# Optimization experiments

Hardware: AMD Instinct MI355X
Metric: run time of the kernel (lower is better)

The kernel has to match this reference:

```python
import jax, jax.numpy as jnp
import numpy as np

N_E = 2048; N_U = 4096; N_SVC = 1024; K = 16; EMB = 8; ED = 8; TH = 16; FD = 32; TK = 3; LVL = 10; B = 8192
DIL = (1, 2, 1, 2)


def setup_inputs() -> dict:
    key = jax.random.key(0)
    ks = list(jax.random.split(key, 64))
    nrm = lambda i, shape, s=0.05: s * jax.random.normal(ks[i], shape, jnp.float32)
    inp = {}
    inp["edge"] = jax.random.normal(ks[0], (1, K, N_E, 11), jnp.float32)
    inp["load"] = jax.random.uniform(ks[1], (1, K, N_E, 3), dtype=jnp.float32)
    inp["svc_tot"] = jax.random.uniform(ks[2], (1, K, N_E, 3), dtype=jnp.float32)
    inp["tra"] = jax.random.normal(ks[3], (1, K, N_U, 4), jnp.float32)
    uid = jax.random.randint(ks[4], (B,), 0, N_U)
    eid = jax.random.randint(ks[5], (B,), 0, N_E)
    sid = jax.random.randint(ks[6], (B,), 0, N_SVC)
    tim = jax.random.randint(ks[7], (B,), 0, K)
    inp["info"] = jnp.stack([uid, eid, sid, tim], -1)[None].astype(jnp.int32)
    inp["srv_attr"] = jnp.concatenate([jnp.arange(N_E)[:, None], jax.random.randint(ks[8], (N_E, 3), 0, LVL)], -1).astype(jnp.int32)
    inp["svc_attr"] = jnp.concatenate([jnp.arange(N_SVC)[:, None], jax.random.randint(ks[9], (N_SVC, 3), 0, LVL)], -1).astype(jnp.int32)
    # --- parameters ---
    inp["usr_tab"] = nrm(10, (N_U, EMB), 1.0)
    inp["srv_tab0"] = nrm(11, (N_E, EMB), 1.0)
    inp["srv_lvl_tabs"] = nrm(12, (3, LVL, EMB), 1.0)
    inp["svc_tab0"] = nrm(13, (N_SVC, EMB), 1.0)
    inp["svc_lvl_tabs"] = nrm(14, (3, LVL, EMB), 1.0)
    inp["lstm_Wih"] = nrm(15, (4 * TH, EMB + 4), 0.2)
    inp["lstm_Whh"] = nrm(16, (4 * TH, TH), 0.2)
    inp["lstm_bih"] = jnp.zeros((4 * TH,), jnp.float32)
    inp["lstm_bhh"] = jnp.zeros((4 * TH,), jnp.float32)
    inp["E1_p"] = nrm(17, (ED, ED, ED), 0.3)
    inp["E2_p"] = nrm(18, (K, ED), 0.01)
    inp["pe_p_W"] = nrm(19, (ED, 11), 0.2)
    inp["pe_p_b"] = jnp.zeros((ED,), jnp.float32)
    inp["E1_a"] = nrm(20, (ED, ED, ED), 0.3)
    inp["E2_a"] = nrm(21, (K, ED), 0.01)
    inp["pe_a_W"] = nrm(22, (ED, 11), 0.2)
    inp["pe_a_b"] = jnp.zeros((ED,), jnp.float32)
    inp["proj_p_W"] = nrm(23, (FD, 3), 0.3)
    inp["proj_p_b"] = jnp.zeros((FD,), jnp.float32)
    inp["proj_a_W"] = nrm(24, (FD, 3), 0.3)
    inp["proj_a_b"] = jnp.zeros((FD,), jnp.float32)
    inp["Wt_p"] = nrm(25, (4, TK, FD, FD), 0.1)
    inp["bt_p"] = jnp.zeros((4, FD), jnp.float32)
    inp["Wg_p"] = nrm(26, (4, FD, FD), 0.1)
    inp["bg_p"] = jnp.zeros((4, FD), jnp.float32)
    inp["Wt_a"] = nrm(27, (4, TK, FD, FD), 0.1)
    inp["bt_a"] = jnp.zeros((4, FD), jnp.float32)
    inp["Wg_a"] = nrm(28, (4, FD, FD), 0.1)
    inp["bg_a"] = jnp.zeros((4, FD), jnp.float32)
    dims = [TH + EMB * 4 * 2 + FD, 64, 32, 16, 8, 4, 1]  # 112 -> ... -> 1
    for i in range(6):
        inp[f"qW{i}"] = nrm(29 + i, (dims[i + 1], dims[i]), 0.1)
        inp[f"qb{i}"] = jnp.zeros((dims[i + 1],), jnp.float32)
    return inp


def _lstm_last(x, Wih, Whh, bih, bhh):
    # x: [n_u, k, in]; returns last hidden state [n_u, TH]
    H = Whh.shape[1]
    def step(carry, xt):
        h, c = carry
        g = xt @ Wih.T + h @ Whh.T + bih + bhh
        i, f, gg, o = jnp.split(g, 4, axis=-1)  # torch gate order i,f,g,o
        c = jax.nn.sigmoid(f) * c + jax.nn.sigmoid(i) * jnp.tanh(gg)
        h = jax.nn.sigmoid(o) * jnp.tanh(c)
        return (h, c), None
    h0 = jnp.zeros((x.shape[0], H), x.dtype)
    (h, _), _ = jax.lax.scan(step, (h0, h0), jnp.swapaxes(x, 0, 1))
    return h


def _adj(ep, E1, E2):
    # einsum('ouv,to,tiu,tjv->tij') factored for efficiency
    M = jnp.einsum('to,ouv->tuv', E2, E1)          # [k, ed, ed]
    T = jnp.einsum('tiu,tuv->tiv', ep, M)          # [k, N, ed]
    S = jnp.einsum('tiv,tjv->tij', T, ep)          # [k, N, N]
    return jax.nn.softmax(jax.nn.relu(S), axis=-1)


def _stream(x, A, Wt, bt, Wg, bg):
    # x: [1, k, N, F]; A: [k, N, N]. Dilated causal temporal conv + graph conv per layer.
    nk = x.shape[1]
    for i, dd in enumerate(DIL):
        pad = (TK - 1) * dd
        xp = jnp.pad(x, ((0, 0), (pad, 0), (0, 0), (0, 0)))
        y = bt[i] + sum(jnp.einsum('btnf,fg->btng', jax.lax.dynamic_slice_in_dim(xp, j * dd, nk, 1), Wt[i, j]) for j in range(TK))
        y = jax.nn.relu(y)
        y = jnp.einsum('btnf,tnm->btmf', y, A)     # per-timestep graph conv
        x = jax.nn.relu(jnp.einsum('btnf,fg->btng', y, Wg[i]) + bg[i])
    return x[:, -1]  # [1, N, F]


def _forward(edge, load, svc_tot, tra, usr_tab, srv_tab0, srv_lvl_tabs, svc_tab0, svc_lvl_tabs,
             lstm_Wih, lstm_Whh, lstm_bih, lstm_bhh,
             E1_p, E2_p, pe_p_W, pe_p_b, E1_a, E2_a, pe_a_W, pe_a_b,
             proj_p_W, proj_p_b, proj_a_W, proj_a_b,
             Wt_p, bt_p, Wg_p, bg_p, Wt_a, bt_a, Wg_a, bg_a,
             qW0, qb0, qW1, qb1, qW2, qb2, qW3, qb3, qW4, qb4, qW5, qb5,
             info, srv_attr, svc_attr):
    edge = edge[0]; loadx = load[0]; svcx = svc_tot[0]; trax = tra[0]; infox = info[0]
    k, n_u = trax.shape[0], trax.shape[1]
    usr_emb = usr_tab[:n_u]                                      # arange lookup
    srv_emb = jnp.concatenate([srv_tab0[srv_attr[:, 0]], srv_lvl_tabs[0][srv_attr[:, 1]],
                               srv_lvl_tabs[1][srv_attr[:, 2]], srv_lvl_tabs[2][srv_attr[:, 3]]], -1)
    svc_emb = jnp.concatenate([svc_tab0[svc_attr[:, 0]], svc_lvl_tabs[0][svc_attr[:, 1]],
                               svc_lvl_tabs[1][svc_attr[:, 2]], svc_lvl_tabs[2][svc_attr[:, 3]]], -1)
    x = jnp.concatenate([jnp.broadcast_to(usr_emb[None], (k, n_u, usr_emb.shape[-1])), trax], -1)
    tra_feat = _lstm_last(jnp.swapaxes(x, 0, 1), lstm_Wih, lstm_Whh, lstm_bih, lstm_bhh)  # [n_u, TH]
    ep = edge @ pe_p_W.T + pe_p_b
    ea = edge @ pe_a_W.T + pe_a_b
    A_p = _adj(ep, E1_p, E2_p)
    A_a = _adj(ea, E1_a, E2_a)
    xp = (loadx @ proj_p_W.T + proj_p_b)[None]   # [1, k, N, FD]
    xa = (svcx @ proj_a_W.T + proj_a_b)[None]
    fp = _stream(xp, A_p, Wt_p, bt_p, Wg_p, bg_p)
    fa = _stream(xa, A_a, Wt_a, bt_a, Wg_a, bg_a)
    srv_fea = (0.5 * (fp + fa))[0]               # mean over stacked streams -> [N, FD]
    h = jnp.concatenate([tra_feat[infox[:, 0]], srv_fea[infox[:, 1]], srv_emb[infox[:, 1]], svc_emb[infox[:, 2]]], -1)
    for W, b in ((qW0, qb0), (qW1, qb1), (qW2, qb2), (qW3, qb3), (qW4, qb4)):
        h = jax.nn.relu(h @ W.T + b)
    return h @ qW5.T + qb5                        # [b, 1]


def reference(edge, load, svc_tot, tra, info, srv_attr, svc_attr, usr_tab, srv_tab0, srv_lvl_tabs, svc_tab0, svc_lvl_tabs,
              lstm_Wih, lstm_Whh, lstm_bih, lstm_bhh,
              E1_p, E2_p, pe_p_W, pe_p_b, E1_a, E2_a, pe_a_W, pe_a_b,
              proj_p_W, proj_p_b, proj_a_W, proj_a_b,
              Wt_p, bt_p, Wg_p, bg_p, Wt_a, bt_a, Wg_a, bg_a,
              qW0, qb0, qW1, qb1, qW2, qb2, qW3, qb3, qW4, qb4, qW5, qb5):
    return _forward(edge, load, svc_tot, tra, usr_tab, srv_tab0, srv_lvl_tabs, svc_tab0, svc_lvl_tabs,
                    lstm_Wih, lstm_Whh, lstm_bih, lstm_bhh,
                    E1_p, E2_p, pe_p_W, pe_p_b, E1_a, E2_a, pe_a_W, pe_a_b,
                    proj_p_W, proj_p_b, proj_a_W, proj_a_b,
                    Wt_p, bt_p, Wg_p, bg_p, Wt_a, bt_a, Wg_a, bg_a,
                    qW0, qb0, qW1, qb1, qW2, qb2, qW3, qb3, qW4, qb4, qW5, qb5,
                    info, srv_attr, svc_attr)
```

## Files before the change

### kernel.cpp

```cpp
#include <hip/hip_runtime.h>
#include <math.h>

#define N_E 2048
#define N_U 4096
#define N_SVC 1024
#define KT 16
#define STRX (KT*N_E*32)
#define YSTR (KT*N_E*32)
#define TSTR (KT*8*N_E)

typedef __attribute__((ext_vector_type(8))) short short8;
typedef __attribute__((ext_vector_type(4))) float f32x4;

__device__ __forceinline__ float sigf(float x){ return 1.0f/(1.0f+__expf(-x)); }
__device__ __forceinline__ float tanhfast(float x){ return 1.0f - 2.0f/(__expf(2.0f*x)+1.0f); }
__device__ __forceinline__ short f2bf(float f){
  union { float f; unsigned u; } x; x.f = f;
  unsigned r = x.u + 0x7FFFu + ((x.u >> 16) & 1u);
  return (short)(r >> 16);
}
__device__ __forceinline__ float bf2f(unsigned short u){
  union { unsigned u; float f; } x; x.u = ((unsigned)u) << 16; return x.f;
}
__device__ __forceinline__ float expm1t(float d){
  float t = fmaf(d, 1.f/24.f, 1.f/6.f);
  t = fmaf(d, t, 0.5f);
  t = fmaf(d, t, 1.f);
  return d*t;
}

__global__ void k_embed(const int* __restrict__ srv_attr, const int* __restrict__ svc_attr,
                        const float* __restrict__ srv_tab0, const float* __restrict__ srv_lvl,
                        const float* __restrict__ svc_tab0, const float* __restrict__ svc_lvl,
                        float* __restrict__ srv_emb, float* __restrict__ svc_emb) {
  int idx = blockIdx.x*256 + threadIdx.x;
  int r = idx >> 5, c = idx & 31;
  int seg = c >> 3, cc = c & 7;
  if (r < N_E) {
    int a = srv_attr[r*4 + seg];
    srv_emb[r*32 + c] = (seg==0) ? srv_tab0[a*8+cc] : srv_lvl[((seg-1)*10 + a)*8 + cc];
  } else {
    int r2 = r - N_E;
    if (r2 < N_SVC) {
      int a = svc_attr[r2*4 + seg];
      svc_emb[r2*32 + c] = (seg==0) ? svc_tab0[a*8+cc] : svc_lvl[((seg-1)*10 + a)*8 + cc];
    }
  }
}

__global__ __launch_bounds__(256) void k_lstm(const float* __restrict__ usr_tab, const float* __restrict__ tra,
                       const float* __restrict__ Wih, const float* __restrict__ Whh,
                       const float* __restrict__ bih, const float* __restrict__ bhh,
                       float* __restrict__ tra_feat) {
  __shared__ float sWih[64*12];
  __shared__ float sWhh[64*16];
  __shared__ float sB[64];
  int tid = threadIdx.x;
  for (int i = tid; i < 64*12; i += 256) sWih[i] = Wih[i];
  for (int i = tid; i < 64*16; i += 256) sWhh[i] = Whh[i];
  if (tid < 64) sB[tid] = bih[tid] + bhh[tid];
  __syncthreads();
  int j  = tid & 15;
  int u  = blockIdx.x*16 + (tid >> 4);
  float xe[8];
  #pragma unroll
  for (int k=0;k<8;k++) xe[k] = usr_tab[u*8+k];
  float h = 0.f, c = 0.f;
  for (int t=0;t<KT;t++) {
    float gi = sB[j], gf = sB[16+j], gg = sB[32+j], go = sB[48+j];
    #pragma unroll
    for (int k=0;k<8;k++) {
      float v = xe[k];
      gi += sWih[j*12+k]*v;      gf += sWih[(16+j)*12+k]*v;
      gg += sWih[(32+j)*12+k]*v; go += sWih[(48+j)*12+k]*v;
    }
    #pragma unroll
    for (int k=0;k<4;k++) {
      float v = tra[((size_t)t*N_U + u)*4 + k];
      gi += sWih[j*12+8+k]*v;      gf += sWih[(16+j)*12+8+k]*v;
      gg += sWih[(32+j)*12+8+k]*v; go += sWih[(48+j)*12+8+k]*v;
    }
    #pragma unroll
    for (int jj=0;jj<16;jj++) {
      float hv = __shfl(h, jj, 16);
      gi += sWhh[j*16+jj]*hv;      gf += sWhh[(16+j)*16+jj]*hv;
      gg += sWhh[(32+j)*16+jj]*hv; go += sWhh[(48+j)*16+jj]*hv;
    }
    c = sigf(gf)*c + sigf(gi)*tanhfast(gg);
    h = sigf(go)*tanhfast(c);
  }
  tra_feat[u*16 + j] = h;
}

__global__ __launch_bounds__(256) void k_peT(const float* __restrict__ edge,
                    const float* __restrict__ Wp, const float* __restrict__ bp,
                    const float* __restrict__ Wa, const float* __restrict__ ba,
                    const float* __restrict__ E1p, const float* __restrict__ E2p,
                    const float* __restrict__ E1a, const float* __restrict__ E2a,
                    float* __restrict__ epp, float* __restrict__ epa,
                    float* __restrict__ Ttp, float* __restrict__ Tta) {
  __shared__ float sM[64];
  __shared__ float sW[88];
  __shared__ float sb[8];
  int s = blockIdx.z, t = 5 + blockIdx.y;
  const float* E1 = s ? E1a : E1p;
  const float* E2 = s ? E2a : E2p;
  const float* W  = s ? Wa : Wp;
  const float* b  = s ? ba : bp;
  float* ep = (s ? epa : epp) + (size_t)t*N_E*8;
  float* Tt = (s ? Tta : Ttp) + (size_t)t*8*N_E;
  int tid = threadIdx.x;
  if (tid < 64) {
    int u = tid >> 3, v = tid & 7;
    float m = 0.f;
    #pragma unroll
    for (int o=0;o<8;o++) m += E2[t*8+o]*E1[(o*8+u)*8+v];
    sM[u*8+v] = m;
  }
  if (tid >= 64 && tid < 152) sW[tid-64] = W[tid-64];
  if (tid >= 152 && tid < 160) sb[tid-152] = b[tid-152];
  __syncthreads();
  int n = blockIdx.x*256 + tid;
  const float* e = edge + ((size_t)t*N_E + n)*11;
  float ev[11];
  #pragma unroll
  for (int k=0;k<11;k++) ev[k] = e[k];
  float epr[8];
  #pragma unroll
  for (int c=0;c<8;c++) {
    float acc = sb[c];
    #pragma unroll
    for (int k=0;k<11;k++) acc = fmaf(ev[k], sW[c*11+k], acc);
    epr[c] = acc;
  }
  float4* eo = (float4*)(ep + (size_t)n*8);
  eo[0] = make_float4(epr[0],epr[1],epr[2],epr[3]);
  eo[1] = make_float4(epr[4],epr[5],epr[6],epr[7]);
  #pragma unroll
  for (int v=0;v<8;v++) {
    float acc = 0.f;
    #pragma unroll
    for (int u=0;u<8;u++) acc = fmaf(epr[u], sM[u*8+v], acc);
    Tt[(size_t)v*N_E + n] = acc;
  }
}

__global__ __launch_bounds__(256) void k_stats(const float* __restrict__ Ttp, const float* __restrict__ Tta,
                        const float* __restrict__ epp, const float* __restrict__ epa,
                        float* __restrict__ partC) {
  __shared__ float sE[256*8];
  int s = blockIdx.z, t = 5 + blockIdx.y;
  int ntile = blockIdx.x & 7, sp = blockIdx.x >> 3;
  int n = ntile*256 + threadIdx.x;
  const float* Tt = (s ? Tta : Ttp) + (size_t)t*8*N_E;
  const float* E = (s ? epa : epp) + (size_t)t*N_E*8;
  int tid = threadIdx.x;
  float tr[8];
  #pragma unroll
  for (int v=0;v<8;v++) tr[v] = Tt[(size_t)v*N_E + n];
  int m0 = sp*256;
  {
    const float4* ge = (const float4*)(E + (size_t)m0*8);
    float4* se = (float4*)sE;
    for (int i = tid; i < 512; i += 256) se[i] = ge[i];
  }
  __syncthreads();
  float qs = 0.f;
  #pragma unroll 4
  for (int m = 0; m < 256; m++) {
    float d = 0.f;
    #pragma unroll
    for (int v=0;v<8;v++) d = fmaf(sE[m*8+v], tr[v], d);
    qs += expm1t(fmaxf(d, 0.f));
  }
  partC[(((size_t)s*KT + t)*8 + sp)*N_E + n] = 256.f + qs;
}

__global__ void k_zinv(const float* __restrict__ partC, float* __restrict__ Z) {
  int i = blockIdx.x*256 + threadIdx.x;
  int n = i & 2047; int stp = i >> 11;
  int s = stp / 11, t = 5 + stp % 11;
  float a = 0.f;
  #pragma unroll
  for (int sp=0;sp<8;sp++) a += partC[(((size_t)s*KT + t)*8 + sp)*N_E + n];
  Z[((size_t)s*KT + t)*N_E + n] = 1.0f/a;
}

__global__ void k_proj(const float* __restrict__ loadx, const float* __restrict__ svcx,
                       const float* __restrict__ Wp, const float* __restrict__ bp,
                       const float* __restrict__ Wa, const float* __restrict__ ba,
                       float* __restrict__ x0p, float* __restrict__ x0a) {
  int idx = blockIdx.x*256 + threadIdx.x;
  int g = idx & 31; int rest = idx >> 5;
  int n = rest & 2047; rest >>= 11; int t = rest & 15; int s = rest >> 4;
  const float* in = (s ? svcx : loadx) + ((size_t)t*N_E + n)*3;
  const float* W = s ? Wa : Wp; const float* b = s ? ba : bp;
  float acc = b[g];
  #pragma unroll
  for (int c=0;c<3;c++) acc += in[c]*W[g*3+c];
  (s ? x0a : x0p)[((size_t)t*N_E + n)*32 + g] = acc;
}

__global__ __launch_bounds__(256) void k_conv(const float* __restrict__ xp, const float* __restrict__ xa,
                       const float* __restrict__ Wtp, const float* __restrict__ Wta,
                       const float* __restrict__ btp, const float* __restrict__ bta,
                       const float* __restrict__ Zg,
                       unsigned short* __restrict__ yp, unsigned short* __restrict__ ya,
                       float* __restrict__ ysumb,
                       int layer, int dd, int tbase, int tstep) {
  __shared__ float sW[3*32*32];
  __shared__ float sX[8][3][32];
  __shared__ float rsum[256];
  int s = blockIdx.z;
  int t = tbase + blockIdx.y*tstep;
  const float* x  = s ? xa : xp;
  const float* Wt = (s ? Wta : Wtp) + (size_t)layer*3*32*32;
  const float* bt = (s ? bta : btp) + layer*32;
  unsigned short* y = s ? ya : yp;
  int tid = threadIdx.x;
  for (int i = tid; i < 3*32*32; i += 256) sW[i] = Wt[i];
  int n0 = blockIdx.x*8;
  for (int i = tid; i < 768; i += 256) {
    int f = i & 31; int nn = (i>>5)&7; int j = i >> 8;
    int tt = t - (2-j)*dd;
    sX[nn][j][f] = (tt >= 0) ? x[((size_t)tt*N_E + n0+nn)*32 + f] : 0.f;
  }
  __syncthreads();
  int g = tid & 31, nn = tid >> 5;
  float acc = bt[g];
  #pragma unroll
  for (int j=0;j<3;j++)
    #pragma unroll
    for (int f=0;f<32;f++) acc += sX[nn][j][f]*sW[(j*32+f)*32+g];
  float zi = Zg[((size_t)s*KT + t)*N_E + n0+nn];
  float val = fmaxf(acc, 0.f)*zi;
  y[((size_t)t*N_E + n0+nn)*32 + g] = (unsigned short)f2bf(val);
  rsum[tid] = val;
  __syncthreads();
  if (tid < 32) {
    float a = 0.f;
    #pragma unroll
    for (int k=0;k<8;k++) a += rsum[tid + 32*k];
    atomicAdd(&ysumb[((size_t)s*gridDim.y + blockIdx.y)*32 + tid], a);
  }
}

__global__ __launch_bounds__(256) void k_mixm(const float* __restrict__ Ttp, const float* __restrict__ Tta,
                      const float* __restrict__ epp, const float* __restrict__ epa,
                      const unsigned short* __restrict__ ybp, const unsigned short* __restrict__ yba,
                      float* __restrict__ part,
                      int tbase, int tstep, int nt, int nsplit) {
  __shared__ float sTt[2][8*132];
  __shared__ unsigned short sYb[2][128*34];
  int s = blockIdx.z, ty = blockIdx.y;
  int t = tbase + ty*tstep;
  int mtile = blockIdx.x & 31, split = blockIdx.x >> 5;
  int tid = threadIdx.x;
  int w = tid >> 6, lane = tid & 63;
  int g = lane >> 4, fc = lane & 15;
  int m0 = mtile*64 + w*16;
  const float* Tt = (s ? Tta : Ttp) + (size_t)t*8*N_E;
  const float* ep = (s ? epa : epp) + (size_t)t*N_E*8;
  const unsigned short* yb = (s ? yba : ybp) + (size_t)t*N_E*32;
  float er[8];
  {
    const float4* gep = (const float4*)(ep + (size_t)(m0 + fc)*8);
    float4 a = gep[0], b = gep[1];
    er[0]=a.x; er[1]=a.y; er[2]=a.z; er[3]=a.w;
    er[4]=b.x; er[5]=b.y; er[6]=b.z; er[7]=b.w;
  }
  f32x4 acc0 = {0.f,0.f,0.f,0.f}, acc1 = {0.f,0.f,0.f,0.f};
  int n0 = split*(N_E/nsplit);
  int nc = (N_E/nsplit)/128;
  int tv = tid >> 5, tc = tid & 31;
  float4 tReg, yR0, yR1;
  {
    tReg = *(const float4*)(Tt + (size_t)tv*N_E + n0 + tc*4);
    const float4* gy = (const float4*)(yb + (size_t)n0*32);
    yR0 = gy[tid]; yR1 = gy[tid + 256];
  }
  for (int ci = 0; ci < nc; ci++) {
    int buf = ci & 1;
    *(float4*)&sTt[buf][tv*132 + tc*4] = tReg;
    {
      union { float4 f; unsigned u[4]; } cv;
      cv.f = yR0;
      unsigned* d0 = (unsigned*)&sYb[buf][(tid>>2)*34 + (tid&3)*8];
      d0[0]=cv.u[0]; d0[1]=cv.u[1]; d0[2]=cv.u[2]; d0[3]=cv.u[3];
      cv.f = yR1;
      unsigned* d1 = (unsigned*)&sYb[buf][(64 + (tid>>2))*34 + (tid&3)*8];
      d1[0]=cv.u[0]; d1[1]=cv.u[1]; d1[2]=cv.u[2]; d1[3]=cv.u[3];
    }
    if (ci + 1 < nc) {
      int c1 = n0 + (ci+1)*128;
      tReg = *(const float4*)(Tt + (size_t)tv*N_E + c1 + tc*4);
      const float4* gy = (const float4*)(yb + (size_t)c1*32);
      yR0 = gy[tid]; yR1 = gy[tid + 256];
    }
    __syncthreads();
    #pragma unroll
    for (int sub = 0; sub < 4; sub++) {
      int rbase = sub*32 + g*8;
      f32x4 dA = {0.f,0.f,0.f,0.f}, dB = {0.f,0.f,0.f,0.f};
      #pragma unroll
      for (int v=0; v<8; v++) {
        const f32x4* tvp = (const f32x4*)&sTt[buf][v*132 + rbase];
        f32x4 ta = tvp[0], tb = tvp[1];
        float e = er[v];
        dA += ta * e;
        dB += tb * e;
      }
      short8 af;
      #pragma unroll
      for (int i=0;i<4;i++) af[i]   = f2bf(expm1t(fmaxf(dA[i], 0.f)));
      #pragma unroll
      for (int i=0;i<4;i++) af[4+i] = f2bf(expm1t(fmaxf(dB[i], 0.f)));
      short8 bf0, bf1;
      #pragma unroll
      for (int i=0;i<8;i++) {
        int row = (rbase + i)*34;
        bf0[i] = (short)sYb[buf][row + fc];
        bf1[i] = (short)sYb[buf][row + 16 + fc];
      }
      acc0 = __builtin_amdgcn_mfma_f32_16x16x32_bf16(af, bf0, acc0, 0, 0, 0);
      acc1 = __builtin_amdgcn_mfma_f32_16x16x32_bf16(af, bf1, acc1, 0, 0, 0);
    }
  }
  float* pb = part + (size_t)((s*nt + ty)*nsplit + split)*(N_E*32);
  #pragma unroll
  for (int r=0;r<4;r++) {
    pb[(size_t)(m0 + g*4 + r)*32 + fc]      = acc0[r];
    pb[(size_t)(m0 + g*4 + r)*32 + 16 + fc] = acc1[r];
  }
}

__global__ __launch_bounds__(256) void k_wg(const float* __restrict__ part,
                     const float* __restrict__ ysumb,
                     const float* __restrict__ Wgp, const float* __restrict__ Wga,
                     const float* __restrict__ bgp, const float* __restrict__ bga,
                     float* __restrict__ xop, float* __restrict__ xoa,
                     int layer, int tbase, int tstep, int nt, int nsplit) {
  __shared__ float sX[8*32];
  __shared__ float sWg[32*32];
  __shared__ float sBg[32];
  int s = blockIdx.z, ty = blockIdx.y;
  int t = tbase + ty*tstep;
  int m0 = blockIdx.x*8;
  const float* Wg = (s ? Wga : Wgp) + (size_t)layer*1024;
  const float* bg = (s ? bga : bgp) + layer*32;
  int tid = threadIdx.x;
  for (int i = tid; i < 1024; i += 256) sWg[i] = Wg[i];
  if (tid < 32) sBg[tid] = bg[tid];
  {
    int mm = tid >> 5, f = tid & 31;
    const float* p = part + (size_t)((s*nt + ty)*nsplit)*(N_E*32) + (size_t)(m0+mm)*32 + f;
    float a = ysumb[((size_t)s*nt + ty)*32 + f];
    for (int sp = 0; sp < nsplit; sp++) a += p[(size_t)sp*(N_E*32)];
    sX[mm*32+f] = a;
  }
  __syncthreads();
  int mm = tid >> 5, g = tid & 31;
  float a = sBg[g];
  #pragma unroll
  for (int f=0;f<32;f++) a += sX[mm*32+f]*sWg[f*32+g];
  (s ? xoa : xop)[((size_t)t*N_E + m0+mm)*32 + g] = fmaxf(a, 0.f);
}

__global__ __launch_bounds__(64) void k_mlp(const int* __restrict__ info,
    const float* __restrict__ tf, const float* __restrict__ fpp, const float* __restrict__ fpa,
    const float* __restrict__ se, const float* __restrict__ ve,
    const float* __restrict__ W0, const float* __restrict__ b0,
    const float* __restrict__ W1, const float* __restrict__ b1,
    const float* __restrict__ W2, const float* __restrict__ b2,
    const float* __restrict__ W3, const float* __restrict__ b3,
    const float* __restrict__ W4, const float* __restrict__ b4,
    const float* __restrict__ W5, const float* __restrict__ b5,
    float* __restrict__ out) {
  __shared__ float sW0t[112*64];
  __shared__ float sW1t[64*32];
  __shared__ float sW2t[32*16];
  __shared__ float sW3t[16*8];
  __shared__ float sW4t[8*4];
  __shared__ float sW5[4];
  __shared__ float sB0[64];
  __shared__ float sB1[32];
  __shared__ float sB2[16];
  __shared__ float sB3[8];
  __shared__ float sB4[4];
  __shared__ float sB5[1];
  int tid = threadIdx.x;
  for (int i = tid; i < 1792; i += 64) {
    float4 v = ((const float4*)W0)[i];
    int g = i / 28, kq = (i % 28)*4;
    sW0t[(kq+0)*64+g]=v.x; sW0t[(kq+1)*64+g]=v.y; sW0t[(kq+2)*64+g]=v.z; sW0t[(kq+3)*64+g]=v.w;
  }
  for (int i = tid; i < 2048; i += 64) sW1t[(i&63)*32 + (i>>6)] = W1[i];
  for (int i = tid; i < 512; i += 64)  sW2t[(i&31)*16 + (i>>5)] = W2[i];
  for (int i = tid; i < 128; i += 64)  sW3t[(i&15)*8  + (i>>4)] = W3[i];
  if (tid < 32) sW4t[(tid&7)*4 + (tid>>3)] = W4[tid];
  if (tid < 4)  sW5[tid] = W5[tid];
  if (tid < 64) sB0[tid] = b0[tid];
  if (tid < 32) sB1[tid] = b1[tid];
  if (tid < 16) sB2[tid] = b2[tid];
  if (tid < 8)  sB3[tid] = b3[tid];
  if (tid < 4)  sB4[tid] = b4[tid];
  if (tid == 0) sB5[0] = b5[0];
  __syncthreads();

  int r = blockIdx.x*64 + tid;
  int4 ifo = ((const int4*)info)[r];
  int uid = ifo.x, eid = ifo.y, sid = ifo.z;

  f32x4 o0v[16];
  #pragma unroll
  for (int gq=0;gq<16;gq++) {
    o0v[gq][0]=sB0[gq*4]; o0v[gq][1]=sB0[gq*4+1]; o0v[gq][2]=sB0[gq*4+2]; o0v[gq][3]=sB0[gq*4+3];
  }
  {
    const float4* p = (const float4*)(tf + (size_t)uid*16);
    #pragma unroll
    for (int q=0;q<4;q++) {
      float4 v4 = p[q];
      #pragma unroll
      for (int j=0;j<4;j++) {
        float v = (&v4.x)[j];
        const f32x4* wc = (const f32x4*)&sW0t[(q*4+j)*64];
        #pragma unroll
        for (int gq=0;gq<16;gq++) o0v[gq] += wc[gq]*v;
      }
    }
  }
  {
    const float4* pp = (const float4*)(fpp + (size_t)eid*32);
    const float4* pa = (const float4*)(fpa + (size_t)eid*32);
    #pragma unroll
    for (int q=0;q<8;q++) {
      float4 a4 = pp[q], b4 = pa[q];
      #pragma unroll
      for (int j=0;j<4;j++) {
        float v = 0.5f*((&a4.x)[j] + (&b4.x)[j]);
        const f32x4* wc = (const f32x4*)&sW0t[(16+q*4+j)*64];
        #pragma unroll
        for (int gq=0;gq<16;gq++) o0v[gq] += wc[gq]*v;
      }
    }
  }
  {
    const float4* p = (const float4*)(se + (size_t)eid*32);
    #pragma unroll
    for (int q=0;q<8;q++) {
      float4 v4 = p[q];
      #pragma unroll
      for (int j=0;j<4;j++) {
        float v = (&v4.x)[j];
        const f32x4* wc = (const f32x4*)&sW0t[(48+q*4+j)*64];
        #pragma unroll
        for (int gq=0;gq<16;gq++) o0v[gq] += wc[gq]*v;
      }
    }
  }
  {
    const float4* p = (const float4*)(ve + (size_t)sid*32);
    #pragma unroll
    for (int q=0;q<8;q++) {
      float4 v4 = p[q];
      #pragma unroll
      for (int j=0;j<4;j++) {
        float v = (&v4.x)[j];
        const f32x4* wc = (const f32x4*)&sW0t[(80+q*4+j)*64];
        #pragma unroll
        for (int gq=0;gq<16;gq++) o0v[gq] += wc[gq]*v;
      }
    }
  }
  #pragma unroll
  for (int gq=0;gq<16;gq++) {
    #pragma unroll
    for (int j=0;j<4;j++) o0v[gq][j] = fmaxf(o0v[gq][j], 0.f);
  }
  f32x4 o1v[8];
  #pragma unroll
  for (int gq=0;gq<8;gq++) {
    o1v[gq][0]=sB1[gq*4]; o1v[gq][1]=sB1[gq*4+1]; o1v[gq][2]=sB1[gq*4+2]; o1v[gq][3]=sB1[gq*4+3];
  }
  #pragma unroll
  for (int k=0;k<64;k++) {
    float v = o0v[k>>2][k&3];
    const f32x4* wc = (const f32x4*)&sW1t[k*32];
    #pragma unroll
    for (int gq=0;gq<8;gq++) o1v[gq] += wc[gq]*v;
  }
  #pragma unroll
  for (int gq=0;gq<8;gq++) {
    #pragma unroll
    for (int j=0;j<4;j++) o1v[gq][j] = fmaxf(o1v[gq][j], 0.f);
  }
  float o2[16];
  #pragma unroll
  for (int g=0;g<16;g++) o2[g] = sB2[g];
  #pragma unroll
  for (int k=0;k<32;k++) {
    float v = o1v[k>>2][k&3];
    #pragma unroll
    for (int g=0;g<16;g++) o2[g] = fmaf(sW2t[k*16+g], v, o2[g]);
  }
  #pragma unroll
  for (int g=0;g<16;g++) o2[g] = fmaxf(o2[g], 0.f);
  float o3[8];
  #pragma unroll
  for (int g=0;g<8;g++) o3[g] = sB3[g];
  #pragma unroll
  for (int k=0;k<16;k++) {
    float v = o2[k];
    #pragma unroll
    for (int g=0;g<8;g++) o3[g] = fmaf(sW3t[k*8+g], v, o3[g]);
  }
  #pragma unroll
  for (int g=0;g<8;g++) o3[g] = fmaxf(o3[g], 0.f);
  float o4[4];
  #pragma unroll
  for (int g=0;g<4;g++) o4[g] = sB4[g];
  #pragma unroll
  for (int k=0;k<8;k++) {
    float v = o3[k];
    #pragma unroll
    for (int g=0;g<4;g++) o4[g] = fmaf(sW4t[k*4+g], v, o4[g]);
  }
  #pragma unroll
  for (int g=0;g<4;g++) o4[g] = fmaxf(o4[g], 0.f);
  float o5 = sB5[0];
  #pragma unroll
  for (int k=0;k<4;k++) o5 = fmaf(sW5[k], o4[k], o5);
  out[r] = o5;
}

extern "C" void kernel_launch(void* const* d_in, const int* in_sizes, int n_in,
                              void* d_out, int out_size, void* d_ws, size_t ws_size,
                              hipStream_t stream) {
  (void)in_sizes; (void)n_in; (void)out_size;
  const float* edge    = (const float*)d_in[0];
  const float* loadx   = (const float*)d_in[1];
  const float* svcx    = (const float*)d_in[2];
  const float* tra     = (const float*)d_in[3];
  const int*   info    = (const int*)d_in[4];
  const int*   srv_attr= (const int*)d_in[5];
  const int*   svc_attr= (const int*)d_in[6];
  const float* usr_tab = (const float*)d_in[7];
  const float* srv_tab0= (const float*)d_in[8];
  const float* srv_lvl = (const float*)d_in[9];
  const float* svc_tab0= (const float*)d_in[10];
  const float* svc_lvl = (const float*)d_in[11];
  const float* Wih = (const float*)d_in[12];
  const float* Whh = (const float*)d_in[13];
  const float* bih = (const float*)d_in[14];
  const float* bhh = (const float*)d_in[15];
  const float* E1p = (const float*)d_in[16];
  const float* E2p = (const float*)d_in[17];
  const float* peWp= (const float*)d_in[18];
  const float* pebp= (const float*)d_in[19];
  const float* E1a = (const float*)d_in[20];
  const float* E2a = (const float*)d_in[21];
  const float* peWa= (const float*)d_in[22];
  const float* peba= (const float*)d_in[23];
  const float* prWp= (const float*)d_in[24];
  const float* prbp= (const float*)d_in[25];
  const float* prWa= (const float*)d_in[26];
  const float* prba= (const float*)d_in[27];
  const float* Wtp = (const float*)d_in[28];
  const float* btp = (const float*)d_in[29];
  const float* Wgp = (const float*)d_in[30];
  const float* bgp = (const float*)d_in[31];
  const float* Wta = (const float*)d_in[32];
  const float* bta = (const float*)d_in[33];
  const float* Wga = (const float*)d_in[34];
  const float* bga = (const float*)d_in[35];
  const float* qW0 = (const float*)d_in[36]; const float* qb0 = (const float*)d_in[37];
  const float* qW1 = (const float*)d_in[38]; const float* qb1 = (const float*)d_in[39];
  const float* qW2 = (const float*)d_in[40]; const float* qb2 = (const float*)d_in[41];
  const float* qW3 = (const float*)d_in[42]; const float* qb3 = (const float*)d_in[43];
  const float* qW4 = (const float*)d_in[44]; const float* qb4 = (const float*)d_in[45];
  const float* qW5 = (const float*)d_in[46]; const float* qb5 = (const float*)d_in[47];
  float* out = (float*)d_out;

  float* ws = (float*)d_ws;
  size_t off = 0;
  float* srv_emb  = ws + off; off += (size_t)N_E*32;
  float* svc_emb  = ws + off; off += (size_t)N_SVC*32;
  float* tra_feat = ws + off; off += (size_t)N_U*16;
  float* epb      = ws + off; off += 2ull*KT*N_E*8;
  float* Ttb      = ws + off; off += 2ull*TSTR;
  float* Zb       = ws + off; off += 2ull*KT*N_E;
  float* ysumb    = ws + off; off += 2ull*KT*32;
  float* x0b      = ws + off; off += 2ull*STRX;
  float* xAb      = ws + off; off += 2ull*STRX;
  unsigned short* ybf = (unsigned short*)(ws + off); off += (2ull*YSTR)/2;
  float* part     = ws + off;

  size_t slab = (size_t)N_E*32;
  size_t avail_floats = (ws_size/4 > off) ? (ws_size/4 - off) : 0;
  int cap = (int)(avail_floats / slab);

  float* epp = epb;              float* epa = epb + (size_t)KT*N_E*8;
  float* Ttp = Ttb;              float* Tta = Ttb + (size_t)TSTR;
  unsigned short* ybp = ybf;     unsigned short* yba = ybf + (size_t)YSTR;
  float* partC = part;

  k_embed<<<384,256,0,stream>>>(srv_attr, svc_attr, srv_tab0, srv_lvl, svc_tab0, svc_lvl, srv_emb, svc_emb);
  k_lstm <<<256,256,0,stream>>>(usr_tab, tra, Wih, Whh, bih, bhh, tra_feat);
  k_peT  <<<dim3(8,11,2),256,0,stream>>>(edge, peWp, pebp, peWa, peba,
                                         E1p, E2p, E1a, E2a, epp, epa, Ttp, Tta);
  k_stats<<<dim3(64,11,2),256,0,stream>>>(Ttp, Tta, epp, epa, partC);
  k_zinv <<<176,256,0,stream>>>(partC, Zb);
  k_proj <<<8192,256,0,stream>>>(loadx, svcx, prWp, prbp, prWa, prba, x0b, x0b + STRX);

  const int Ldd[4]   = {1, 2, 1, 2};
  const int Ltb[4]   = {5, 9, 11, 15};
  const int Lts[4]   = {1, 1, 2, 1};
  const int Lnt[4]   = {11, 7, 3, 1};
  int Lsp[4]         = {4, 4, 8, 16};
  for (int i = 0; i < 4; i++)
    while (Lsp[i] > 1 && 2*Lnt[i]*Lsp[i] > cap) Lsp[i] >>= 1;

  float* xin = x0b;
  float* xout = xAb;
  for (int i = 0; i < 4; i++) {
    hipMemsetAsync(ysumb, 0, 2ull*KT*32*sizeof(float), stream);
    k_conv<<<dim3(256, Lnt[i], 2), 256, 0, stream>>>(
        xin, xin + STRX, Wtp, Wta, btp, bta, Zb, ybp, yba, ysumb, i, Ldd[i], Ltb[i], Lts[i]);
    k_mixm<<<dim3(32*Lsp[i], Lnt[i], 2), 256, 0, stream>>>(
        Ttp, Tta, epp, epa, ybp, yba, part, Ltb[i], Lts[i], Lnt[i], Lsp[i]);
    k_wg<<<dim3(256, Lnt[i], 2), 256, 0, stream>>>(
        part, ysumb, Wgp, Wga, bgp, bga, xout, xout + STRX, i, Ltb[i], Lts[i], Lnt[i], Lsp[i]);
    float* tmp = xin; xin = xout; xout = tmp;
  }
  const float* fpp = xin + (size_t)15*N_E*32;
  const float* fpa = xin + STRX + (size_t)15*N_E*32;

  k_mlp<<<128,64,0,stream>>>(info, tra_feat, fpp, fpa, srv_emb, svc_emb,
                             qW0, qb0, qW1, qb1, qW2, qb2, qW3, qb3, qW4, qb4, qW5, qb5, out);
}
```

Before: 488.5 us.

## Fuse projection and Z-normalization into neighbors, widen mixm M-tile, drop per-layer memsets

The input projection (k_proj) now runs inside the layer-0 conv, which computes projected features straight from load/svc inputs, so the full x0 tensor is never written or read. k_zinv is removed: k_stats accumulates its partial row sums into Z with atomics, and the conv takes the reciprocal on the fly. Per-layer ysum buffers are cleared by a single upfront memset, replacing four memsets inside the layer loop. k_mixm now handles 128 rows per block with two sets of A fragments, reusing the B fragments loaded from LDS across twice as many MFMAs. The costs are higher register pressure in mixm, fewer blocks per launch, and atomic contention in k_stats.

```diff
diff --git a/kernel.cpp b/kernel.cpp
--- a/kernel.cpp
+++ b/kernel.cpp
@@ -147,7 +147,7 @@
 
 __global__ __launch_bounds__(256) void k_stats(const float* __restrict__ Ttp, const float* __restrict__ Tta,
                         const float* __restrict__ epp, const float* __restrict__ epa,
-                        float* __restrict__ partC) {
+                        float* __restrict__ Zb) {
   __shared__ float sE[256*8];
   int s = blockIdx.z, t = 5 + blockIdx.y;
   int ntile = blockIdx.x & 7, sp = blockIdx.x >> 3;
@@ -173,44 +173,24 @@
     for (int v=0;v<8;v++) d = fmaf(sE[m*8+v], tr[v], d);
     qs += expm1t(fmaxf(d, 0.f));
   }
-  partC[(((size_t)s*KT + t)*8 + sp)*N_E + n] = 256.f + qs;
-}
-
-__global__ void k_zinv(const float* __restrict__ partC, float* __restrict__ Z) {
-  int i = blockIdx.x*256 + threadIdx.x;
-  int n = i & 2047; int stp = i >> 11;
-  int s = stp / 11, t = 5 + stp % 11;
-  float a = 0.f;
-  #pragma unroll
-  for (int sp=0;sp<8;sp++) a += partC[(((size_t)s*KT + t)*8 + sp)*N_E + n];
-  Z[((size_t)s*KT + t)*N_E + n] = 1.0f/a;
-}
-
-__global__ void k_proj(const float* __restrict__ loadx, const float* __restrict__ svcx,
-                       const float* __restrict__ Wp, const float* __restrict__ bp,
-                       const float* __restrict__ Wa, const float* __restrict__ ba,
-                       float* __restrict__ x0p, float* __restrict__ x0a) {
-  int idx = blockIdx.x*256 + threadIdx.x;
-  int g = idx & 31; int rest = idx >> 5;
-  int n = rest & 2047; rest >>= 11; int t = rest & 15; int s = rest >> 4;
-  const float* in = (s ? svcx : loadx) + ((size_t)t*N_E + n)*3;
-  const float* W = s ? Wa : Wp; const float* b = s ? ba : bp;
-  float acc = b[g];
-  #pragma unroll
-  for (int c=0;c<3;c++) acc += in[c]*W[g*3+c];
-  (s ? x0a : x0p)[((size_t)t*N_E + n)*32 + g] = acc;
+  atomicAdd(&Zb[((size_t)s*KT + t)*N_E + n], 256.f + qs);
 }
 
 __global__ __launch_bounds__(256) void k_conv(const float* __restrict__ xp, const float* __restrict__ xa,
+                       const float* __restrict__ loadx, const float* __restrict__ svcx,
+                       const float* __restrict__ prWp, const float* __restrict__ prbp,
+                       const float* __restrict__ prWa, const float* __restrict__ prba,
                        const float* __restrict__ Wtp, const float* __restrict__ Wta,
                        const float* __restrict__ btp, const float* __restrict__ bta,
                        const float* __restrict__ Zg,
                        unsigned short* __restrict__ yp, unsigned short* __restrict__ ya,
-                       float* __restrict__ ysumb,
+                       float* __restrict__ ysumL,
                        int layer, int dd, int tbase, int tstep) {
   __shared__ float sW[3*32*32];
   __shared__ float sX[8][3][32];
   __shared__ float rsum[256];
+  __shared__ float sPW[96];
+  __shared__ float sPb[32];
   int s = blockIdx.z;
   int t = tbase + blockIdx.y*tstep;
   const float* x  = s ? xa : xp;
@@ -218,12 +198,34 @@
   const float* bt = (s ? bta : btp) + layer*32;
   unsigned short* y = s ? ya : yp;
   int tid = threadIdx.x;
+  if (layer == 0) {
+    if (tid < 96) sPW[tid] = (s ? prWa : prWp)[tid];
+    else if (tid < 128) sPb[tid-96] = (s ? prba : prbp)[tid-96];
+    __syncthreads();
+  }
   for (int i = tid; i < 3*32*32; i += 256) sW[i] = Wt[i];
   int n0 = blockIdx.x*8;
-  for (int i = tid; i < 768; i += 256) {
-    int f = i & 31; int nn = (i>>5)&7; int j = i >> 8;
-    int tt = t - (2-j)*dd;
-    sX[nn][j][f] = (tt >= 0) ? x[((size_t)tt*N_E + n0+nn)*32 + f] : 0.f;
+  if (layer == 0) {
+    const float* inx = s ? svcx : loadx;
+    for (int i = tid; i < 768; i += 256) {
+      int f = i & 31; int nn = (i>>5)&7; int j = i >> 8;
+      int tt = t - (2-j)*dd;
+      float v = 0.f;
+      if (tt >= 0) {
+        const float* ip = inx + ((size_t)tt*N_E + n0+nn)*3;
+        v = sPb[f];
+        v = fmaf(ip[0], sPW[f*3+0], v);
+        v = fmaf(ip[1], sPW[f*3+1], v);
+        v = fmaf(ip[2], sPW[f*3+2], v);
+      }
+      sX[nn][j][f] = v;
+    }
+  } else {
+    for (int i = tid; i < 768; i += 256) {
+      int f = i & 31; int nn = (i>>5)&7; int j = i >> 8;
+      int tt = t - (2-j)*dd;
+      sX[nn][j][f] = (tt >= 0) ? x[((size_t)tt*N_E + n0+nn)*32 + f] : 0.f;
+    }
   }
   __syncthreads();
   int g = tid & 31, nn = tid >> 5;
@@ -232,7 +234,7 @@
   for (int j=0;j<3;j++)
     #pragma unroll
     for (int f=0;f<32;f++) acc += sX[nn][j][f]*sW[(j*32+f)*32+g];
-  float zi = Zg[((size_t)s*KT + t)*N_E + n0+nn];
+  float zi = 1.0f / Zg[((size_t)s*KT + t)*N_E + n0+nn];
   float val = fmaxf(acc, 0.f)*zi;
   y[((size_t)t*N_E + n0+nn)*32 + g] = (unsigned short)f2bf(val);
   rsum[tid] = val;
@@ -241,7 +243,7 @@
     float a = 0.f;
     #pragma unroll
     for (int k=0;k<8;k++) a += rsum[tid + 32*k];
-    atomicAdd(&ysumb[((size_t)s*gridDim.y + blockIdx.y)*32 + tid], a);
+    atomicAdd(&ysumL[((size_t)s*gridDim.y + blockIdx.y)*32 + tid], a);
   }
 }
 
@@ -254,22 +256,27 @@
   __shared__ unsigned short sYb[2][128*34];
   int s = blockIdx.z, ty = blockIdx.y;
   int t = tbase + ty*tstep;
-  int mtile = blockIdx.x & 31, split = blockIdx.x >> 5;
+  int mtile = blockIdx.x & 15, split = blockIdx.x >> 4;
   int tid = threadIdx.x;
   int w = tid >> 6, lane = tid & 63;
   int g = lane >> 4, fc = lane & 15;
-  int m0 = mtile*64 + w*16;
+  int m0 = mtile*128 + w*16;
   const float* Tt = (s ? Tta : Ttp) + (size_t)t*8*N_E;
   const float* ep = (s ? epa : epp) + (size_t)t*N_E*8;
   const unsigned short* yb = (s ? yba : ybp) + (size_t)t*N_E*32;
-  float er[8];
+  float er0[8], er1[8];
   {
     const float4* gep = (const float4*)(ep + (size_t)(m0 + fc)*8);
     float4 a = gep[0], b = gep[1];
-    er[0]=a.x; er[1]=a.y; er[2]=a.z; er[3]=a.w;
-    er[4]=b.x; er[5]=b.y; er[6]=b.z; er[7]=b.w;
-  }
-  f32x4 acc0 = {0.f,0.f,0.f,0.f}, acc1 = {0.f,0.f,0.f,0.f};
+    er0[0]=a.x; er0[1]=a.y; er0[2]=a.z; er0[3]=a.w;
+    er0[4]=b.x; er0[5]=b.y; er0[6]=b.z; er0[7]=b.w;
+    const float4* gep1 = (const float4*)(ep + (size_t)(m0 + 64 + fc)*8);
+    float4 c = gep1[0], d = gep1[1];
+    er1[0]=c.x; er1[1]=c.y; er1[2]=c.z; er1[3]=c.w;
+    er1[4]=d.x; er1[5]=d.y; er1[6]=d.z; er1[7]=d.w;
+  }
+  f32x4 accA0 = {0.f,0.f,0.f,0.f}, accA1 = {0.f,0.f,0.f,0.f};
+  f32x4 accB0 = {0.f,0.f,0.f,0.f}, accB1 = {0.f,0.f,0.f,0.f};
   int n0 = split*(N_E/nsplit);
   int nc = (N_E/nsplit)/128;
   int tv = tid >> 5, tc = tid & 31;
@@ -301,20 +308,25 @@
     #pragma unroll
     for (int sub = 0; sub < 4; sub++) {
       int rbase = sub*32 + g*8;
-      f32x4 dA = {0.f,0.f,0.f,0.f}, dB = {0.f,0.f,0.f,0.f};
+      f32x4 dA0 = {0.f,0.f,0.f,0.f}, dB0 = {0.f,0.f,0.f,0.f};
+      f32x4 dA1 = {0.f,0.f,0.f,0.f}, dB1 = {0.f,0.f,0.f,0.f};
       #pragma unroll
       for (int v=0; v<8; v++) {
         const f32x4* tvp = (const f32x4*)&sTt[buf][v*132 + rbase];
         f32x4 ta = tvp[0], tb = tvp[1];
-        float e = er[v];
-        dA += ta * e;
-        dB += tb * e;
+        float e0 = er0[v], e1 = er1[v];
+        dA0 += ta * e0;  dB0 += tb * e0;
+        dA1 += ta * e1;  dB1 += tb * e1;
       }
-      short8 af;
-      #pragma unroll
-      for (int i=0;i<4;i++) af[i]   = f2bf(expm1t(fmaxf(dA[i], 0.f)));
-      #pragma unroll
-      for (int i=0;i<4;i++) af[4+i] = f2bf(expm1t(fmaxf(dB[i], 0.f)));
+      short8 af0, af1;
+      #pragma unroll
+      for (int i=0;i<4;i++) af0[i]   = f2bf(expm1t(fmaxf(dA0[i], 0.f)));
+      #pragma unroll
+      for (int i=0;i<4;i++) af0[4+i] = f2bf(expm1t(fmaxf(dB0[i], 0.f)));
+      #pragma unroll
+      for (int i=0;i<4;i++) af1[i]   = f2bf(expm1t(fmaxf(dA1[i], 0.f)));
+      #pragma unroll
+      for (int i=0;i<4;i++) af1[4+i] = f2bf(expm1t(fmaxf(dB1[i], 0.f)));
       short8 bf0, bf1;
       #pragma unroll
       for (int i=0;i<8;i++) {
@@ -322,20 +334,24 @@
         bf0[i] = (short)sYb[buf][row + fc];
         bf1[i] = (short)sYb[buf][row + 16 + fc];
       }
-      acc0 = __builtin_amdgcn_mfma_f32_16x16x32_bf16(af, bf0, acc0, 0, 0, 0);
-      acc1 = __builtin_amdgcn_mfma_f32_16x16x32_bf16(af, bf1, acc1, 0, 0, 0);
+      accA0 = __builtin_amdgcn_mfma_f32_16x16x32_bf16(af0, bf0, accA0, 0, 0, 0);
+      accA1 = __builtin_amdgcn_mfma_f32_16x16x32_bf16(af0, bf1, accA1, 0, 0, 0);
+      accB0 = __builtin_amdgcn_mfma_f32_16x16x32_bf16(af1, bf0, accB0, 0, 0, 0);
+      accB1 = __builtin_amdgcn_mfma_f32_16x16x32_bf16(af1, bf1, accB1, 0, 0, 0);
     }
   }
   float* pb = part + (size_t)((s*nt + ty)*nsplit + split)*(N_E*32);
   #pragma unroll
   for (int r=0;r<4;r++) {
-    pb[(size_t)(m0 + g*4 + r)*32 + fc]      = acc0[r];
-    pb[(size_t)(m0 + g*4 + r)*32 + 16 + fc] = acc1[r];
+    pb[(size_t)(m0 + g*4 + r)*32 + fc]           = accA0[r];
+    pb[(size_t)(m0 + g*4 + r)*32 + 16 + fc]      = accA1[r];
+    pb[(size_t)(m0 + 64 + g*4 + r)*32 + fc]      = accB0[r];
+    pb[(size_t)(m0 + 64 + g*4 + r)*32 + 16 + fc] = accB1[r];
   }
 }
 
 __global__ __launch_bounds__(256) void k_wg(const float* __restrict__ part,
-                     const float* __restrict__ ysumb,
+                     const float* __restrict__ ysumL,
                      const float* __restrict__ Wgp, const float* __restrict__ Wga,
                      const float* __restrict__ bgp, const float* __restrict__ bga,
                      float* __restrict__ xop, float* __restrict__ xoa,
@@ -354,7 +370,7 @@
   {
     int mm = tid >> 5, f = tid & 31;
     const float* p = part + (size_t)((s*nt + ty)*nsplit)*(N_E*32) + (size_t)(m0+mm)*32 + f;
-    float a = ysumb[((size_t)s*nt + ty)*32 + f];
+    float a = ysumL[((size_t)s*nt + ty)*32 + f];
     for (int sp = 0; sp < nsplit; sp++) a += p[(size_t)sp*(N_E*32)];
     sX[mm*32+f] = a;
   }
@@ -590,9 +606,10 @@
   float* epb      = ws + off; off += 2ull*KT*N_E*8;
   float* Ttb      = ws + off; off += 2ull*TSTR;
   float* Zb       = ws + off; off += 2ull*KT*N_E;
-  float* ysumb    = ws + off; off += 2ull*KT*32;
-  float* x0b      = ws + off; off += 2ull*STRX;
-  float* xAb      = ws + off; off += 2ull*STRX;
+  float* ysumb    = ws + off; off += 4ull*2*11*32;
+  size_t zclr_bytes = (2ull*KT*N_E + 4ull*2*11*32)*4;
+  float* xA       = ws + off; off += 2ull*STRX;
+  float* xB       = ws + off; off += 2ull*STRX;
   unsigned short* ybf = (unsigned short*)(ws + off); off += (2ull*YSTR)/2;
   float* part     = ws + off;
 
@@ -603,15 +620,13 @@
   float* epp = epb;              float* epa = epb + (size_t)KT*N_E*8;
   float* Ttp = Ttb;              float* Tta = Ttb + (size_t)TSTR;
   unsigned short* ybp = ybf;     unsigned short* yba = ybf + (size_t)YSTR;
-  float* partC = part;
-
+
+  hipMemsetAsync(Zb, 0, zclr_bytes, stream);
   k_embed<<<384,256,0,stream>>>(srv_attr, svc_attr, srv_tab0, srv_lvl, svc_tab0, svc_lvl, srv_emb, svc_emb);
   k_lstm <<<256,256,0,stream>>>(usr_tab, tra, Wih, Whh, bih, bhh, tra_feat);
   k_peT  <<<dim3(8,11,2),256,0,stream>>>(edge, peWp, pebp, peWa, peba,
                                          E1p, E2p, E1a, E2a, epp, epa, Ttp, Tta);
-  k_stats<<<dim3(64,11,2),256,0,stream>>>(Ttp, Tta, epp, epa, partC);
-  k_zinv <<<176,256,0,stream>>>(partC, Zb);
-  k_proj <<<8192,256,0,stream>>>(loadx, svcx, prWp, prbp, prWa, prba, x0b, x0b + STRX);
+  k_stats<<<dim3(64,11,2),256,0,stream>>>(Ttp, Tta, epp, epa, Zb);
 
   const int Ldd[4]   = {1, 2, 1, 2};
   const int Ltb[4]   = {5, 9, 11, 15};
@@ -621,20 +636,20 @@
   for (int i = 0; i < 4; i++)
     while (Lsp[i] > 1 && 2*Lnt[i]*Lsp[i] > cap) Lsp[i] >>= 1;
 
-  float* xin = x0b;
-  float* xout = xAb;
+  const float* convin[4] = {xA , xA, xB, xA};
+  float*       wgout[4]  = {xA, xB, xA, xB};
   for (int i = 0; i < 4; i++) {
-    hipMemsetAsync(ysumb, 0, 2ull*KT*32*sizeof(float), stream);
+    float* ysumL = ysumb + (size_t)i*2*11*32;
     k_conv<<<dim3(256, Lnt[i], 2), 256, 0, stream>>>(
-        xin, xin + STRX, Wtp, Wta, btp, bta, Zb, ybp, yba, ysumb, i, Ldd[i], Ltb[i], Lts[i]);
-    k_mixm<<<dim3(32*Lsp[i], Lnt[i], 2), 256, 0, stream>>>(
+        convin[i], convin[i] + STRX, loadx, svcx, prWp, prbp, prWa, prba,
+        Wtp, Wta, btp, bta, Zb, ybp, yba, ysumL, i, Ldd[i], Ltb[i], Lts[i]);
+    k_mixm<<<dim3(16*Lsp[i], Lnt[i], 2), 256, 0, stream>>>(
         Ttp, Tta, epp, epa, ybp, yba, part, Ltb[i], Lts[i], Lnt[i], Lsp[i]);
     k_wg<<<dim3(256, Lnt[i], 2), 256, 0, stream>>>(
-        part, ysumb, Wgp, Wga, bgp, bga, xout, xout + STRX, i, Ltb[i], Lts[i], Lnt[i], Lsp[i]);
-    float* tmp = xin; xin = xout; xout = tmp;
-  }
-  const float* fpp = xin + (size_t)15*N_E*32;
-  const float* fpa = xin + STRX + (size_t)15*N_E*32;
+        part, ysumL, Wgp, Wga, bgp, bga, wgout[i], wgout[i] + STRX, i, Ltb[i], Lts[i], Lnt[i], Lsp[i]);
+  }
+  const float* fpp = xB + (size_t)15*N_E*32;
+  const float* fpa = xB + STRX + (size_t)15*N_E*32;
 
   k_mlp<<<128,64,0,stream>>>(info, tra_feat, fpp, fpa, srv_emb, svc_emb,
                              qW0, qb0, qW1, qb1, qW2, qb2, qW3, qb3, qW4, qb4, qW5, qb5, out);
```

After: 471.8 us. -3.4%, faster.
